# Performance work log

Measured on AMD Instinct MI355X. Metric: run time of the kernel, lower is better.

Reference implementation:

```python
import jax, jax.numpy as jnp
import numpy as np

B, S, HID = 1, 2048, 2880
H, HKV, D = 64, 8, 64
WINDOW = 128
SCALE = D ** -0.5
NEG = -1e30


def _rope(x, cos, sin):
    # x: [B, S, h, D]; cos/sin: [S, D//2]; interleaved complex rotation
    x1 = x[..., 0::2]
    x2 = x[..., 1::2]
    c = cos[None, :, None, :]
    s = sin[None, :, None, :]
    o1 = x1 * c - x2 * s
    o2 = x1 * s + x2 * c
    out = jnp.stack([o1, o2], axis=-1)  # [B,S,h,D/2,2]
    return out.reshape(x.shape)


def setup_inputs() -> dict:
    key = jax.random.key(0)
    ks = jax.random.split(key, 12)
    x = jax.random.normal(ks[0], (B, S, HID), dtype=jnp.float32)
    # rotary tables (head_dim/2 frequencies)
    inv_freq = 1.0 / (10000.0 ** (np.arange(0, D, 2, dtype=np.float32) / D))
    t = np.arange(S, dtype=np.float32)
    ang = np.outer(t, inv_freq)  # [S, D/2]
    cos = jnp.asarray(np.cos(ang))
    sin = jnp.asarray(np.sin(ang))
    std = 0.02
    Wq = jax.random.normal(ks[1], (HID, H * D), dtype=jnp.float32) * std
    bq = jnp.zeros((H * D,), dtype=jnp.float32)
    Wk = jax.random.normal(ks[2], (HID, HKV * D), dtype=jnp.float32) * std
    bk = jnp.zeros((HKV * D,), dtype=jnp.float32)
    Wv = jax.random.normal(ks[3], (HID, HKV * D), dtype=jnp.float32) * std
    bv = jnp.zeros((HKV * D,), dtype=jnp.float32)
    Wo = jax.random.normal(ks[4], (H * D, HID), dtype=jnp.float32) * std
    bo = jnp.zeros((HID,), dtype=jnp.float32)
    sinks = jax.random.normal(ks[5], (H,), dtype=jnp.float32) * std
    return {"x": x, "cos": cos, "sin": sin, "Wq": Wq, "bq": bq,
            "Wk": Wk, "bk": bk, "Wv": Wv, "bv": bv, "Wo": Wo, "bo": bo,
            "sinks": sinks}


def reference(x, cos, sin, Wq, bq, Wk, bk, Wv, bv, Wo, bo, sinks):
    b, s, _ = x.shape
    q = (x @ Wq + bq).reshape(b, s, H, D)
    k = (x @ Wk + bk).reshape(b, s, HKV, D)
    v = (x @ Wv + bv).reshape(b, s, HKV, D)
    q = _rope(q, cos, sin)
    k = _rope(k, cos, sin)
    # GQA: expand kv heads to H
    rep = H // HKV
    k = jnp.repeat(k, rep, axis=2)  # [B,S,H,D]
    v = jnp.repeat(v, rep, axis=2)
    scores = jnp.einsum("bqhd,bkhd->bhqk", q, k) * SCALE  # [B,H,S,S]
    i = jnp.arange(s)[:, None]
    j = jnp.arange(s)[None, :]
    mask = (j <= i) & (i - j < WINDOW)  # causal sliding window
    z = jnp.where(mask[None, None], scores, NEG)
    sink = sinks[None, :, None]  # [1,H,1] extra logit per head
    m = jnp.maximum(jnp.max(z, axis=-1), sink)  # [B,H,S]
    p = jnp.exp(z - m[..., None])
    denom = jnp.sum(p, axis=-1) + jnp.exp(sink - m)  # [B,H,S]
    out = jnp.einsum("bhqk,bkhd->bhqd", p, v) / denom[..., None]
    out = out.transpose(0, 2, 1, 3).reshape(b, s, H * D)
    return out @ Wo + bo
```

## Files before the change

### kernel.cpp

```cpp
#include <hip/hip_runtime.h>
#include <stdint.h>

#define S_LEN   2048
#define HID_DIM 2880
#define NHEAD   64
#define NKVH    8
#define DHEAD   64
#define NQ      4096
#define NKVD    512
#define NQKV    5120
#define WOPAD   2944
#define ATT_SCALE 0.125f
#define NEGINF  (-1e30f)

typedef __attribute__((ext_vector_type(8))) short bf16x8;
typedef __attribute__((ext_vector_type(4))) float f32x4;

typedef __attribute__((address_space(3))) uint32_t lds_u32;
typedef const __attribute__((address_space(1))) uint32_t glb_u32;

__device__ __forceinline__ void gl_lds16(const short* g, short* l) {
  __builtin_amdgcn_global_load_lds((glb_u32*)(uintptr_t)g,
                                   (lds_u32*)(uint32_t)(uintptr_t)l, 16, 0, 0);
}

__device__ __forceinline__ short f2bf(float f) {
  union { float f; uint32_t u; } c; c.f = f;
  uint32_t u = c.u;
  return (short)((u + 0x7FFFu + ((u >> 16) & 1u)) >> 16);
}

__global__ void k_cvt_x(const float* __restrict__ src, short* __restrict__ dst, int n4) {
  int i = blockIdx.x * 256 + threadIdx.x;
  if (i >= n4) return;
  float4 v = ((const float4*)src)[i];
  short4 o;
  o.x = f2bf(v.x); o.y = f2bf(v.y); o.z = f2bf(v.z); o.w = f2bf(v.w);
  ((short4*)dst)[i] = o;
}

__global__ void k_transpose_cvt(const float* __restrict__ src, short* __restrict__ dst,
                                int K, int N) {
  __shared__ float tile[32][33];
  int k0 = blockIdx.x * 32, n0 = blockIdx.y * 32;
  int tx = threadIdx.x, ty = threadIdx.y;
#pragma unroll
  for (int j = 0; j < 4; ++j) {
    int n = n0 + tx, k = k0 + ty + j * 8;
    tile[ty + j * 8][tx] = (n < N) ? src[(size_t)k * N + n] : 0.f;
  }
  __syncthreads();
#pragma unroll
  for (int j = 0; j < 4; ++j) {
    int n = n0 + ty + j * 8;
    dst[(size_t)n * K + k0 + tx] = f2bf(tile[tx][ty + j * 8]);
  }
}

template <int EPI>
__global__ __launch_bounds__(256) void k_gemm(
    const short* __restrict__ A, const short* __restrict__ B, int K,
    const float* __restrict__ biasq, const float* __restrict__ biask,
    const float* __restrict__ biasv,
    const float* __restrict__ cosT, const float* __restrict__ sinT,
    short* __restrict__ qout, short* __restrict__ kout, short* __restrict__ vout,
    const float* __restrict__ bo, float* __restrict__ out) {
  const int tid = threadIdx.x;
  const int lane = tid & 63, wid = tid >> 6;
  const int wm = wid >> 1, wn = wid & 1;
  const int l15 = lane & 15, lhi = lane >> 4;
  const int row0 = blockIdx.y * 128, col0 = blockIdx.x * 128;

  __shared__ short As[128 * 64];
  __shared__ short Bs[128 * 64];

  f32x4 acc[4][4];
#pragma unroll
  for (int i = 0; i < 4; ++i)
#pragma unroll
    for (int j = 0; j < 4; ++j) acc[i][j] = (f32x4){0.f, 0.f, 0.f, 0.f};

  const short* aSrc[4];
  const short* bSrc[4];
  short* aDst[4];
  short* bDst[4];
#pragma unroll
  for (int i = 0; i < 4; ++i) {
    int p = i * 256 + tid;
    int m = p >> 3, slot = p & 7;
    int ss = slot ^ (m & 7);
    aSrc[i] = A + (size_t)(row0 + m) * K + ss * 8;
    bSrc[i] = B + (size_t)(col0 + m) * K + ss * 8;
    aDst[i] = As + p * 8;
    bDst[i] = Bs + p * 8;
  }

  const int nkt = K >> 6;
  for (int kt = 0; kt < nkt; ++kt) {
    __syncthreads();
#pragma unroll
    for (int i = 0; i < 4; ++i) gl_lds16(aSrc[i] + kt * 64, aDst[i]);
#pragma unroll
    for (int i = 0; i < 4; ++i) gl_lds16(bSrc[i] + kt * 64, bDst[i]);
    __syncthreads();
#pragma unroll
    for (int kk = 0; kk < 2; ++kk) {
      bf16x8 af[4], bf[4];
#pragma unroll
      for (int mi = 0; mi < 4; ++mi) {
        int r = wm * 64 + mi * 16 + l15;
        int sl = (kk * 4 + lhi) ^ (r & 7);
        af[mi] = *(const bf16x8*)((char*)As + r * 128 + sl * 16);
      }
#pragma unroll
      for (int ni = 0; ni < 4; ++ni) {
        int r = wn * 64 + ni * 16 + l15;
        int sl = (kk * 4 + lhi) ^ (r & 7);
        bf[ni] = *(const bf16x8*)((char*)Bs + r * 128 + sl * 16);
      }
#pragma unroll
      for (int mi = 0; mi < 4; ++mi)
#pragma unroll
        for (int ni = 0; ni < 4; ++ni)
          acc[mi][ni] = __builtin_amdgcn_mfma_f32_16x16x32_bf16(af[mi], bf[ni], acc[mi][ni], 0, 0, 0);
    }
  }

  if (EPI == 0) {
#pragma unroll
    for (int mi = 0; mi < 4; ++mi) {
#pragma unroll
      for (int r = 0; r < 4; ++r) {
        int mg = row0 + wm * 64 + mi * 16 + lhi * 4 + r;
#pragma unroll
        for (int ni = 0; ni < 4; ++ni) {
          int ng = col0 + wn * 64 + ni * 16 + l15;
          float v = acc[mi][ni][r];
          v += (ng < NQ) ? biasq[ng] : (ng < NQ + NKVD ? biask[ng - NQ] : biasv[ng - NQ - NKVD]);
          if (ng < NQ + NKVD) {
            float partner = __shfl_xor(v, 1);
            int d = ng & 63, p = d >> 1;
            float c = cosT[mg * 32 + p], s = sinT[mg * 32 + p];
            v = (d & 1) ? (partner * s + v * c) : (v * c - partner * s);
          }
          short b16 = f2bf(v);
          if (ng < NQ)              qout[(size_t)mg * NQ + ng] = b16;
          else if (ng < NQ + NKVD)  kout[(size_t)mg * NKVD + (ng - NQ)] = b16;
          else                      vout[(size_t)mg * NKVD + (ng - NQ - NKVD)] = b16;
        }
      }
    }
  } else {
#pragma unroll
    for (int mi = 0; mi < 4; ++mi) {
#pragma unroll
      for (int r = 0; r < 4; ++r) {
        int mg = row0 + wm * 64 + mi * 16 + lhi * 4 + r;
#pragma unroll
        for (int ni = 0; ni < 4; ++ni) {
          int ng = col0 + wn * 64 + ni * 16 + l15;
          if (ng < HID_DIM) out[(size_t)mg * HID_DIM + ng] = acc[mi][ni][r] + bo[ng];
        }
      }
    }
  }
}

__global__ __launch_bounds__(256) void k_attn(
    const short* __restrict__ qb, const short* __restrict__ kb,
    const short* __restrict__ vb, const float* __restrict__ sinks,
    short* __restrict__ attnb) {
  const int h = blockIdx.x & 63;
  const int q0 = (blockIdx.x >> 6) * 64;
  const int tid = threadIdx.x;
  const int lane = tid & 63, wq = tid >> 6;
  const int l15 = lane & 15, lhi = lane >> 4;
  const int hkv = h >> 3;
  const int kstart = q0 - 128;

  __shared__ short Vt[64 * 256];
  __shared__ short Plds[4][16 * 168];

  {
    int d = tid >> 2;
    int k16 = (tid & 3) * 16;
#pragma unroll
    for (int j = 0; j < 16; j += 4)
      *(short4*)&Vt[d * 256 + 192 + k16 + j] = (short4){0, 0, 0, 0};
  }

  {
    int krow = tid >> 2;
    int dbase = (tid & 3) * 16;
#pragma unroll
    for (int rep = 0; rep < 3; ++rep) {
      int key = rep * 64 + krow;
      int gk = kstart + key;
      int gkc = gk < 0 ? 0 : gk;
      const short* src = vb + (size_t)gkc * NKVD + hkv * 64 + dbase;
      uint4 v0 = *(const uint4*)(src);
      uint4 v1 = *(const uint4*)(src + 8);
      uint32_t w[8] = {v0.x, v0.y, v0.z, v0.w, v1.x, v1.y, v1.z, v1.w};
#pragma unroll
      for (int i = 0; i < 8; ++i) {
        int d0 = dbase + 2 * i, d1 = dbase + 2 * i + 1;
        Vt[d0 * 256 + (key ^ ((d0 & 7) << 3))] = (short)(w[i] & 0xffffu);
        Vt[d1 * 256 + (key ^ ((d1 & 7) << 3))] = (short)(w[i] >> 16);
      }
    }
  }

  int qrow = q0 + wq * 16 + l15;
  bf16x8 aq[2];
#pragma unroll
  for (int kk = 0; kk < 2; ++kk)
    aq[kk] = *(const bf16x8*)(qb + (size_t)qrow * NQ + h * 64 + kk * 32 + lhi * 8);

  f32x4 sacc[9];
#pragma unroll
  for (int ni = 0; ni < 9; ++ni) {
    int key = kstart + (wq + ni) * 16 + l15;
    int keyc = key < 0 ? 0 : key;
    const short* kp = kb + (size_t)keyc * NKVD + hkv * 64;
    bf16x8 b0 = *(const bf16x8*)(kp + lhi * 8);
    bf16x8 b1 = *(const bf16x8*)(kp + 32 + lhi * 8);
    f32x4 z = (f32x4){0.f, 0.f, 0.f, 0.f};
    z = __builtin_amdgcn_mfma_f32_16x16x32_bf16(aq[0], b0, z, 0, 0, 0);
    z = __builtin_amdgcn_mfma_f32_16x16x32_bf16(aq[1], b1, z, 0, 0, 0);
    sacc[ni] = z;
  }

  float snk = sinks[h];
  float mx[4] = {NEGINF, NEGINF, NEGINF, NEGINF};
#pragma unroll
  for (int ni = 0; ni < 9; ++ni) {
    int j = kstart + (wq + ni) * 16 + l15;
#pragma unroll
    for (int r = 0; r < 4; ++r) {
      int iq = q0 + wq * 16 + lhi * 4 + r;
      float sv = sacc[ni][r] * ATT_SCALE;
      bool valid = (j >= 0) && (j <= iq) && (iq - j < 128);
      sv = valid ? sv : NEGINF;
      sacc[ni][r] = sv;
      mx[r] = fmaxf(mx[r], sv);
    }
  }
#pragma unroll
  for (int r = 0; r < 4; ++r) {
    float m = mx[r];
    m = fmaxf(m, __shfl_xor(m, 1));
    m = fmaxf(m, __shfl_xor(m, 2));
    m = fmaxf(m, __shfl_xor(m, 4));
    m = fmaxf(m, __shfl_xor(m, 8));
    mx[r] = fmaxf(m, snk);
  }
  float sm[4] = {0.f, 0.f, 0.f, 0.f};
#pragma unroll
  for (int ni = 0; ni < 9; ++ni)
#pragma unroll
    for (int r = 0; r < 4; ++r) {
      float p = __expf(sacc[ni][r] - mx[r]);
      sacc[ni][r] = p;
      sm[r] += p;
    }
  float inv[4];
#pragma unroll
  for (int r = 0; r < 4; ++r) {
    float s = sm[r];
    s += __shfl_xor(s, 1);
    s += __shfl_xor(s, 2);
    s += __shfl_xor(s, 4);
    s += __shfl_xor(s, 8);
    s += __expf(snk - mx[r]);
    inv[r] = 1.0f / s;
  }

  short* pw = &Plds[wq][0];
#pragma unroll
  for (int ni = 0; ni < 9; ++ni)
#pragma unroll
    for (int r = 0; r < 4; ++r)
      pw[(lhi * 4 + r) * 168 + ni * 16 + l15] = f2bf(sacc[ni][r]);
#pragma unroll
  for (int r = 0; r < 4; ++r)
    pw[(lhi * 4 + r) * 168 + 144 + l15] = 0;

  __syncthreads();

  f32x4 oacc[4];
#pragma unroll
  for (int nt = 0; nt < 4; ++nt) oacc[nt] = (f32x4){0.f, 0.f, 0.f, 0.f};
  const short* pr = &Plds[wq][0];
#pragma unroll
  for (int ks = 0; ks < 5; ++ks) {
    bf16x8 pf = *(const bf16x8*)(pr + l15 * 168 + ks * 32 + lhi * 8);
#pragma unroll
    for (int nt = 0; nt < 4; ++nt) {
      int d = nt * 16 + l15;
      int keyidx = wq * 16 + ks * 32 + lhi * 8;
      bf16x8 vf = *(const bf16x8*)(&Vt[d * 256 + (keyidx ^ ((d & 7) << 3))]);
      oacc[nt] = __builtin_amdgcn_mfma_f32_16x16x32_bf16(pf, vf, oacc[nt], 0, 0, 0);
    }
  }

#pragma unroll
  for (int nt = 0; nt < 4; ++nt)
#pragma unroll
    for (int r = 0; r < 4; ++r) {
      int iq = q0 + wq * 16 + lhi * 4 + r;
      int d = nt * 16 + l15;
      attnb[(size_t)iq * NQ + h * 64 + d] = f2bf(oacc[nt][r] * inv[r]);
    }
}

extern "C" void kernel_launch(void* const* d_in, const int* in_sizes, int n_in,
                              void* d_out, int out_size, void* d_ws, size_t ws_size,
                              hipStream_t stream) {
  const float* x     = (const float*)d_in[0];
  const float* cosT  = (const float*)d_in[1];
  const float* sinT  = (const float*)d_in[2];
  const float* Wq    = (const float*)d_in[3];
  const float* bq    = (const float*)d_in[4];
  const float* Wk    = (const float*)d_in[5];
  const float* bk    = (const float*)d_in[6];
  const float* Wv    = (const float*)d_in[7];
  const float* bv    = (const float*)d_in[8];
  const float* Wo    = (const float*)d_in[9];
  const float* bo    = (const float*)d_in[10];
  const float* sinks = (const float*)d_in[11];
  float* out = (float*)d_out;

  short* xb    = (short*)d_ws;
  short* wqkvb = xb + (size_t)S_LEN * HID_DIM;
  short* wob   = wqkvb + (size_t)NQKV * HID_DIM;
  short* qbuf  = wob + (size_t)WOPAD * NQ;
  short* kbuf  = qbuf + (size_t)S_LEN * NQ;
  short* vbuf  = kbuf + (size_t)S_LEN * NKVD;
  short* attnb = vbuf + (size_t)S_LEN * NKVD;

  dim3 tb(32, 8);
  k_cvt_x<<<(S_LEN * HID_DIM / 4 + 255) / 256, 256, 0, stream>>>(x, xb, S_LEN * HID_DIM / 4);
  k_transpose_cvt<<<dim3(HID_DIM / 32, NQ / 32), tb, 0, stream>>>(Wq, wqkvb, HID_DIM, NQ);
  k_transpose_cvt<<<dim3(HID_DIM / 32, NKVD / 32), tb, 0, stream>>>(Wk, wqkvb + (size_t)NQ * HID_DIM, HID_DIM, NKVD);
  k_transpose_cvt<<<dim3(HID_DIM / 32, NKVD / 32), tb, 0, stream>>>(Wv, wqkvb + (size_t)(NQ + NKVD) * HID_DIM, HID_DIM, NKVD);
  k_transpose_cvt<<<dim3(NQ / 32, WOPAD / 32), tb, 0, stream>>>(Wo, wob, NQ, HID_DIM);

  k_gemm<0><<<dim3(NQKV / 128, S_LEN / 128), 256, 0, stream>>>(
      xb, wqkvb, HID_DIM, bq, bk, bv, cosT, sinT, qbuf, kbuf, vbuf, nullptr, nullptr);

  k_attn<<<(S_LEN / 64) * NHEAD, 256, 0, stream>>>(qbuf, kbuf, vbuf, sinks, attnb);

  k_gemm<1><<<dim3(WOPAD / 128, S_LEN / 128), 256, 0, stream>>>(
      attnb, wob, NQ, nullptr, nullptr, nullptr, nullptr, nullptr,
      nullptr, nullptr, nullptr, bo, out);
}
```

Measured before the change: 254.6 us.

## Double-buffer GEMM LDS tiles with async global-to-LDS prefetch

Splits the GEMM's shared-memory A/B tiles into two buffers. The next K-tile is prefetched with global_load_lds into the idle buffer while MFMAs consume the current one, and a partial vmcnt wait replaces the full sync before each compute step. The aim is to hide global load latency behind matrix math. In exchange it doubles LDS use per block (64KB), which may cut occupancy, and it relies on hand-placed waitcnt/barrier ordering for correctness.

```diff
diff --git a/kernel.cpp b/kernel.cpp
--- a/kernel.cpp
+++ b/kernel.cpp
@@ -71,8 +71,8 @@
   const int l15 = lane & 15, lhi = lane >> 4;
   const int row0 = blockIdx.y * 128, col0 = blockIdx.x * 128;
 
-  __shared__ short As[128 * 64];
-  __shared__ short Bs[128 * 64];
+  __shared__ short As[2][128 * 64];
+  __shared__ short Bs[2][128 * 64];
 
   f32x4 acc[4][4];
 #pragma unroll
@@ -82,8 +82,7 @@
 
   const short* aSrc[4];
   const short* bSrc[4];
-  short* aDst[4];
-  short* bDst[4];
+  int dOff[4];
 #pragma unroll
   for (int i = 0; i < 4; ++i) {
     int p = i * 256 + tid;
@@ -91,18 +90,29 @@
     int ss = slot ^ (m & 7);
     aSrc[i] = A + (size_t)(row0 + m) * K + ss * 8;
     bSrc[i] = B + (size_t)(col0 + m) * K + ss * 8;
-    aDst[i] = As + p * 8;
-    bDst[i] = Bs + p * 8;
+    dOff[i] = p * 8;
   }
 
   const int nkt = K >> 6;
+
+#pragma unroll
+  for (int i = 0; i < 4; ++i) gl_lds16(aSrc[i], &As[0][dOff[i]]);
+#pragma unroll
+  for (int i = 0; i < 4; ++i) gl_lds16(bSrc[i], &Bs[0][dOff[i]]);
+
   for (int kt = 0; kt < nkt; ++kt) {
-    __syncthreads();
-#pragma unroll
-    for (int i = 0; i < 4; ++i) gl_lds16(aSrc[i] + kt * 64, aDst[i]);
-#pragma unroll
-    for (int i = 0; i < 4; ++i) gl_lds16(bSrc[i] + kt * 64, bDst[i]);
-    __syncthreads();
+    const int cur = kt & 1;
+    __builtin_amdgcn_s_barrier();
+    if (kt + 1 < nkt) {
+#pragma unroll
+      for (int i = 0; i < 4; ++i) gl_lds16(aSrc[i] + (kt + 1) * 64, &As[cur ^ 1][dOff[i]]);
+#pragma unroll
+      for (int i = 0; i < 4; ++i) gl_lds16(bSrc[i] + (kt + 1) * 64, &Bs[cur ^ 1][dOff[i]]);
+      asm volatile("s_waitcnt vmcnt(8)" ::: "memory");
+    } else {
+      asm volatile("s_waitcnt vmcnt(0)" ::: "memory");
+    }
+    __builtin_amdgcn_s_barrier();
 #pragma unroll
     for (int kk = 0; kk < 2; ++kk) {
       bf16x8 af[4], bf[4];
@@ -110,13 +120,13 @@
       for (int mi = 0; mi < 4; ++mi) {
         int r = wm * 64 + mi * 16 + l15;
         int sl = (kk * 4 + lhi) ^ (r & 7);
-        af[mi] = *(const bf16x8*)((char*)As + r * 128 + sl * 16);
+        af[mi] = *(const bf16x8*)((char*)&As[cur][0] + r * 128 + sl * 16);
       }
 #pragma unroll
       for (int ni = 0; ni < 4; ++ni) {
         int r = wn * 64 + ni * 16 + l15;
         int sl = (kk * 4 + lhi) ^ (r & 7);
-        bf[ni] = *(const bf16x8*)((char*)Bs + r * 128 + sl * 16);
+        bf[ni] = *(const bf16x8*)((char*)&Bs[cur][0] + r * 128 + sl * 16);
       }
 #pragma unroll
       for (int mi = 0; mi < 4; ++mi)
```

Measured after the change: 273.7 us. 7.5% more time.
